# Optimization experiments

Measured on AMD Instinct MI355X. Metric: run time of the kernel, lower is better.

## Reference

```python
import jax, jax.numpy as jnp
import numpy as np

NUM_VIEWS = 24
SLOPE = 0.2
P = 14 * 14  # 196 spatial features per view
OUT = 1024


def setup_inputs() -> dict:
    key = jax.random.key(0)
    ks = jax.random.split(key, 6)
    B = 16384
    x = jax.random.normal(ks[0], (B, 14, 14, NUM_VIEWS), dtype=jnp.float32)
    indices = jax.random.randint(ks[1], (NUM_VIEWS,), 0, NUM_VIEWS, dtype=jnp.int64)
    # fc_idx: Linear(num_views -> 196); fc_aggre: Linear(392 -> 1024)
    W_idx = jax.random.normal(ks[2], (P, NUM_VIEWS), dtype=jnp.float32) * (1.0 / np.sqrt(NUM_VIEWS))
    b_idx = jax.random.normal(ks[3], (P,), dtype=jnp.float32) * 0.01
    W_aggre = jax.random.normal(ks[4], (OUT, 2 * P), dtype=jnp.float32) * (1.0 / np.sqrt(2 * P))
    b_aggre = jax.random.normal(ks[5], (OUT,), dtype=jnp.float32) * 0.01
    return {"x": x, "indices": indices, "W_idx": W_idx, "b_idx": b_idx,
            "W_aggre": W_aggre, "b_aggre": b_aggre}


def reference(x, indices, W_idx, b_idx, W_aggre, b_aggre):
    B, s1, s2, s3 = x.shape
    K = indices.shape[0]
    xr = x.reshape(B, s1 * s2, s3)            # [B, 196, V]
    # one-hot index path is batch-independent: compute once per idx
    oh = jax.nn.one_hot(indices, s3, dtype=x.dtype)                # [K, V]
    infer_index = jax.nn.leaky_relu(oh @ W_idx.T + b_idx, SLOPE)   # [K, 196]
    x_sel = jnp.take(xr, indices, axis=2)                          # [B, 196, K]
    # fc_aggre(cat(x_part, idx_part)) summed over K, split weight by halves
    Wx = W_aggre[:, :s1 * s2]   # [1024, 196] acts on x part
    Wi = W_aggre[:, s1 * s2:]   # [1024, 196] acts on index part
    out_x = jnp.einsum('bpk,op->bo', x_sel, Wx)                    # [B, 1024]
    out_i = infer_index.sum(axis=0) @ Wi.T                         # [1024]
    out = out_x + out_i + K * b_aggre                              # broadcast over batch
    return out
```

## Files before the change

### kernel.cpp

```cpp
#include <hip/hip_runtime.h>

#define B_ROWS 16384
#define PDIM 196
#define KPAD 224
#define NV 24
#define OUT_DIM 1024
#define SLOPE 0.2f

typedef __attribute__((ext_vector_type(8))) short short8;
typedef __attribute__((ext_vector_type(4))) float floatx4;

static __device__ __forceinline__ unsigned short f2bf(float f) {
    union { float f; unsigned int u; } v; v.f = f;
    unsigned int r = v.u + 0x7fffu + ((v.u >> 16) & 1u);
    return (unsigned short)(r >> 16);
}

__global__ void const_kernel(const int* __restrict__ idx,
                             const float* __restrict__ W_idx,
                             const float* __restrict__ b_idx,
                             const float* __restrict__ W_aggre,
                             const float* __restrict__ b_aggre,
                             float* __restrict__ cvec) {
    __shared__ float v_sh[PDIM];
    __shared__ int idx_sh[NV];
    int t = threadIdx.x;
    if (t < NV) idx_sh[t] = idx[t];
    __syncthreads();
    if (t < PDIM) {
        float bp = b_idx[t];
        float a = 0.f;
        for (int k = 0; k < NV; ++k) {
            float z = W_idx[t * NV + idx_sh[k]] + bp;
            a += (z > 0.f) ? z : SLOPE * z;
        }
        v_sh[t] = a;
    }
    __syncthreads();
    for (int o = t; o < OUT_DIM; o += 256) {
        float a = (float)NV * b_aggre[o];
        const float* wr = W_aggre + (size_t)o * (2 * PDIM) + PDIM;
        for (int p = 0; p < PDIM; ++p) a += v_sh[p] * wr[p];
        cvec[o] = a;
    }
}

__global__ void pack_b(const float* __restrict__ W_aggre,
                       unsigned short* __restrict__ Bp) {
    int tid = blockIdx.x * blockDim.x + threadIdx.x;
    if (tid >= 7 * 64 * 64) return;
    int ks = tid >> 12;
    int rem = tid & 4095;
    int nt = rem >> 6;
    int lane = rem & 63;
    int n = nt * 16 + (lane & 15);
    int kb = ks * 32 + (lane >> 4) * 8;
    unsigned short* dst = Bp + (size_t)tid * 8;
    for (int j = 0; j < 8; ++j) {
        int k = kb + j;
        float v = (k < PDIM) ? W_aggre[(size_t)n * (2 * PDIM) + k] : 0.f;
        dst[j] = f2bf(v);
    }
}

__global__ __launch_bounds__(256) void reduce_x(const float* __restrict__ x,
                                                const int* __restrict__ idx,
                                                unsigned short* __restrict__ Sm) {
    __shared__ float scnt[NV];
    int t = threadIdx.x;
    if (t < NV) {
        int c = 0;
        for (int k = 0; k < NV; ++k) c += (idx[k] == t);
        scnt[t] = (float)c;
    }
    __syncthreads();
    long g = (long)blockIdx.x * 256 + t;
    int b = (int)(g / KPAD);
    int p = (int)(g - (long)b * KPAD);
    float a = 0.f;
    if (p < PDIM) {
        const float4* x4 = (const float4*)(x + ((size_t)b * PDIM + p) * NV);
        #pragma unroll
        for (int i = 0; i < 6; ++i) {
            float4 q = x4[i];
            a += scnt[4 * i + 0] * q.x + scnt[4 * i + 1] * q.y +
                 scnt[4 * i + 2] * q.z + scnt[4 * i + 3] * q.w;
        }
        Sm[g] = f2bf(a);
    } else {
        Sm[g] = 0;
    }
}

__global__ __launch_bounds__(256) void gemm_k(const unsigned short* __restrict__ Sm,
                                              const unsigned short* __restrict__ Bp,
                                              const float* __restrict__ cvec,
                                              float* __restrict__ out) {
    int tid = threadIdx.x;
    int lane = tid & 63, wave = tid >> 6;
    int wm = wave >> 1, wn = wave & 1;
    int quad = lane >> 4, l15 = lane & 15;
    int bm = blockIdx.y, bn = blockIdx.x;

    floatx4 acc[4][4];
    #pragma unroll
    for (int i = 0; i < 4; ++i)
        #pragma unroll
        for (int j = 0; j < 4; ++j)
            acc[i][j] = (floatx4){0.f, 0.f, 0.f, 0.f};

    int arow = bm * 128 + wm * 64 + l15;
    int ntg0 = bn * 8 + wn * 4;

    #pragma unroll
    for (int ks = 0; ks < 7; ++ks) {
        short8 af[4], bfr[4];
        #pragma unroll
        for (int mt = 0; mt < 4; ++mt) {
            const unsigned short* ap =
                Sm + (size_t)(arow + mt * 16) * KPAD + ks * 32 + quad * 8;
            af[mt] = *(const short8*)ap;
        }
        #pragma unroll
        for (int nt = 0; nt < 4; ++nt) {
            const unsigned short* bp =
                Bp + ((size_t)((ks * 64 + ntg0 + nt) * 64 + lane)) * 8;
            bfr[nt] = *(const short8*)bp;
        }
        #pragma unroll
        for (int mt = 0; mt < 4; ++mt)
            #pragma unroll
            for (int nt = 0; nt < 4; ++nt)
                acc[mt][nt] = __builtin_amdgcn_mfma_f32_16x16x32_bf16(
                    af[mt], bfr[nt], acc[mt][nt], 0, 0, 0);
    }

    int colb = bn * 128 + wn * 64 + l15;
    #pragma unroll
    for (int nt = 0; nt < 4; ++nt) {
        float cv = cvec[colb + nt * 16];
        #pragma unroll
        for (int mt = 0; mt < 4; ++mt) {
            int row0 = bm * 128 + wm * 64 + mt * 16 + quad * 4;
            float* po = out + (size_t)row0 * OUT_DIM + colb + nt * 16;
            po[0 * OUT_DIM] = acc[mt][nt][0] + cv;
            po[1 * OUT_DIM] = acc[mt][nt][1] + cv;
            po[2 * OUT_DIM] = acc[mt][nt][2] + cv;
            po[3 * OUT_DIM] = acc[mt][nt][3] + cv;
        }
    }
}

extern "C" void kernel_launch(void* const* d_in, const int* in_sizes, int n_in,
                              void* d_out, int out_size, void* d_ws, size_t ws_size,
                              hipStream_t stream) {
    const float* x       = (const float*)d_in[0];
    const int*   idx     = (const int*)d_in[1];
    const float* W_idx   = (const float*)d_in[2];
    const float* b_idx   = (const float*)d_in[3];
    const float* W_aggre = (const float*)d_in[4];
    const float* b_aggre = (const float*)d_in[5];
    float* out = (float*)d_out;

    char* ws = (char*)d_ws;
    float*          cvec = (float*)ws;
    unsigned short* Bp   = (unsigned short*)(ws + 4096);
    unsigned short* Sm   = (unsigned short*)(ws + 524288);

    hipLaunchKernelGGL(const_kernel, dim3(1), dim3(256), 0, stream,
                       idx, W_idx, b_idx, W_aggre, b_aggre, cvec);
    hipLaunchKernelGGL(pack_b, dim3(112), dim3(256), 0, stream, W_aggre, Bp);
    hipLaunchKernelGGL(reduce_x, dim3(B_ROWS * KPAD / 256), dim3(256), 0, stream,
                       x, idx, Sm);
    hipLaunchKernelGGL(gemm_k, dim3(8, 128), dim3(256), 0, stream,
                       Sm, Bp, cvec, out);
}
```

Baseline: 514.1 us.

## Merge prep kernels, parallelize cvec, and pre-swizzle Sm into MFMA fragment layout

Combines the weight-packing and constant-vector kernels into one launch and spreads the cvec dot products across 32 blocks, using 8-lane shuffle reductions instead of a single block of serial loops. The reduction kernel now writes the bf16 A operand directly in MFMA fragment order, so each gemm lane reads one contiguous 16-byte chunk per tile. This is meant to cut launch overhead, the single-block serial bottleneck, and strided A loads. In exchange, the reduce kernel's stores become scattered.

```diff
diff --git a/kernel.cpp b/kernel.cpp
--- a/kernel.cpp
+++ b/kernel.cpp
@@ -16,50 +16,56 @@
     return (unsigned short)(r >> 16);
 }
 
-__global__ void const_kernel(const int* __restrict__ idx,
-                             const float* __restrict__ W_idx,
-                             const float* __restrict__ b_idx,
-                             const float* __restrict__ W_aggre,
-                             const float* __restrict__ b_aggre,
-                             float* __restrict__ cvec) {
-    __shared__ float v_sh[PDIM];
-    __shared__ int idx_sh[NV];
+__global__ __launch_bounds__(256) void prep_kernel(
+        const int* __restrict__ idx,
+        const float* __restrict__ W_idx,
+        const float* __restrict__ b_idx,
+        const float* __restrict__ W_aggre,
+        const float* __restrict__ b_aggre,
+        unsigned short* __restrict__ Bp,
+        float* __restrict__ cvec) {
     int t = threadIdx.x;
-    if (t < NV) idx_sh[t] = idx[t];
-    __syncthreads();
-    if (t < PDIM) {
-        float bp = b_idx[t];
+    if (blockIdx.x < 112) {
+        int tid = blockIdx.x * 256 + t;
+        int ks = tid >> 12;
+        int rem = tid & 4095;
+        int nt = rem >> 6;
+        int lane = rem & 63;
+        int n = nt * 16 + (lane & 15);
+        int kb = ks * 32 + (lane >> 4) * 8;
+        unsigned short* dst = Bp + (size_t)tid * 8;
+        #pragma unroll
+        for (int j = 0; j < 8; ++j) {
+            int k = kb + j;
+            float v = (k < PDIM) ? W_aggre[(size_t)n * (2 * PDIM) + k] : 0.f;
+            dst[j] = f2bf(v);
+        }
+    } else {
+        __shared__ float v_sh[PDIM];
+        __shared__ int idx_sh[NV];
+        if (t < NV) idx_sh[t] = idx[t];
+        __syncthreads();
+        if (t < PDIM) {
+            float bp = b_idx[t];
+            float a = 0.f;
+            #pragma unroll
+            for (int k = 0; k < NV; ++k) {
+                float z = W_idx[t * NV + idx_sh[k]] + bp;
+                a += (z > 0.f) ? z : SLOPE * z;
+            }
+            v_sh[t] = a;
+        }
+        __syncthreads();
+        int bc = blockIdx.x - 112;
+        int o = bc * 32 + (t >> 3);
+        int pl = t & 7;
+        const float* wr = W_aggre + (size_t)o * (2 * PDIM) + PDIM;
         float a = 0.f;
-        for (int k = 0; k < NV; ++k) {
-            float z = W_idx[t * NV + idx_sh[k]] + bp;
-            a += (z > 0.f) ? z : SLOPE * z;
-        }
-        v_sh[t] = a;
-    }
-    __syncthreads();
-    for (int o = t; o < OUT_DIM; o += 256) {
-        float a = (float)NV * b_aggre[o];
-        const float* wr = W_aggre + (size_t)o * (2 * PDIM) + PDIM;
-        for (int p = 0; p < PDIM; ++p) a += v_sh[p] * wr[p];
-        cvec[o] = a;
-    }
-}
-
-__global__ void pack_b(const float* __restrict__ W_aggre,
-                       unsigned short* __restrict__ Bp) {
-    int tid = blockIdx.x * blockDim.x + threadIdx.x;
-    if (tid >= 7 * 64 * 64) return;
-    int ks = tid >> 12;
-    int rem = tid & 4095;
-    int nt = rem >> 6;
-    int lane = rem & 63;
-    int n = nt * 16 + (lane & 15);
-    int kb = ks * 32 + (lane >> 4) * 8;
-    unsigned short* dst = Bp + (size_t)tid * 8;
-    for (int j = 0; j < 8; ++j) {
-        int k = kb + j;
-        float v = (k < PDIM) ? W_aggre[(size_t)n * (2 * PDIM) + k] : 0.f;
-        dst[j] = f2bf(v);
+        for (int p = pl; p < PDIM; p += 8) a += v_sh[p] * wr[p];
+        a += __shfl_down(a, 4, 8);
+        a += __shfl_down(a, 2, 8);
+        a += __shfl_down(a, 1, 8);
+        if (pl == 0) cvec[o] = a + (float)NV * b_aggre[o];
     }
 }
 
@@ -70,26 +76,28 @@
     int t = threadIdx.x;
     if (t < NV) {
         int c = 0;
+        #pragma unroll
         for (int k = 0; k < NV; ++k) c += (idx[k] == t);
         scnt[t] = (float)c;
     }
     __syncthreads();
-    long g = (long)blockIdx.x * 256 + t;
-    int b = (int)(g / KPAD);
-    int p = (int)(g - (long)b * KPAD);
+    unsigned g = blockIdx.x * 256u + t;
+    unsigned row = g / KPAD;
+    unsigned p = g - row * KPAD;
     float a = 0.f;
     if (p < PDIM) {
-        const float4* x4 = (const float4*)(x + ((size_t)b * PDIM + p) * NV);
+        const float4* x4 = (const float4*)(x + ((size_t)row * PDIM + p) * NV);
         #pragma unroll
         for (int i = 0; i < 6; ++i) {
             float4 q = x4[i];
             a += scnt[4 * i + 0] * q.x + scnt[4 * i + 1] * q.y +
                  scnt[4 * i + 2] * q.z + scnt[4 * i + 3] * q.w;
         }
-        Sm[g] = f2bf(a);
-    } else {
-        Sm[g] = 0;
     }
+    unsigned rt = row >> 4, l15 = row & 15;
+    unsigned ks = p >> 5, quad = (p >> 3) & 3, j = p & 7;
+    size_t addr = (((size_t)rt * 7 + ks) * 64 + quad * 16 + l15) * 8 + j;
+    Sm[addr] = (p < PDIM) ? f2bf(a) : (unsigned short)0;
 }
 
 __global__ __launch_bounds__(256) void gemm_k(const unsigned short* __restrict__ Sm,
@@ -109,7 +117,7 @@
         for (int j = 0; j < 4; ++j)
             acc[i][j] = (floatx4){0.f, 0.f, 0.f, 0.f};
 
-    int arow = bm * 128 + wm * 64 + l15;
+    int rt0 = bm * 8 + wm * 4;
     int ntg0 = bn * 8 + wn * 4;
 
     #pragma unroll
@@ -118,7 +126,7 @@
         #pragma unroll
         for (int mt = 0; mt < 4; ++mt) {
             const unsigned short* ap =
-                Sm + (size_t)(arow + mt * 16) * KPAD + ks * 32 + quad * 8;
+                Sm + (((size_t)(rt0 + mt) * 7 + ks) * 64 + lane) * 8;
             af[mt] = *(const short8*)ap;
         }
         #pragma unroll
@@ -141,7 +149,7 @@
         float cv = cvec[colb + nt * 16];
         #pragma unroll
         for (int mt = 0; mt < 4; ++mt) {
-            int row0 = bm * 128 + wm * 64 + mt * 16 + quad * 4;
+            int row0 = (rt0 + mt) * 16 + quad * 4;
             float* po = out + (size_t)row0 * OUT_DIM + colb + nt * 16;
             po[0 * OUT_DIM] = acc[mt][nt][0] + cv;
             po[1 * OUT_DIM] = acc[mt][nt][1] + cv;
@@ -167,9 +175,8 @@
     unsigned short* Bp   = (unsigned short*)(ws + 4096);
     unsigned short* Sm   = (unsigned short*)(ws + 524288);
 
-    hipLaunchKernelGGL(const_kernel, dim3(1), dim3(256), 0, stream,
-                       idx, W_idx, b_idx, W_aggre, b_aggre, cvec);
-    hipLaunchKernelGGL(pack_b, dim3(112), dim3(256), 0, stream, W_aggre, Bp);
+    hipLaunchKernelGGL(prep_kernel, dim3(144), dim3(256), 0, stream,
+                       idx, W_idx, b_idx, W_aggre, b_aggre, Bp, cvec);
     hipLaunchKernelGGL(reduce_x, dim3(B_ROWS * KPAD / 256), dim3(256), 0, stream,
                        x, idx, Sm);
     hipLaunchKernelGGL(gemm_k, dim3(8, 128), dim3(256), 0, stream,
```

New measurement: 466.8 us. 9.2% less time.
